# Kernel tuning notes

Hardware: AMD Instinct MI355X
Metric: run time of the kernel (lower is better)

## Reference

```python
import jax, jax.numpy as jnp
import numpy as np

FRAME_PERIOD = 80   # samples per frame
IR_LENGTH = 2000    # filter length L (taps = L-1)
N_FFT = 4096


def setup_inputs() -> dict:
    key = jax.random.key(0)
    k1, k2 = jax.random.split(key)
    x = jax.random.normal(k1, (2, 24000), dtype=jnp.float32)          # waveform, T = 300*80
    mc = jax.random.normal(k2, (2, 300, 25), dtype=jnp.float32) * 0.1  # mel-cepstrum (B, N, M+1)
    return {"x": x, "mc": mc}


def _c2min_phase_ir(c):
    # cepstrum -> minimum-phase impulse response: ifft(exp(fft(c))) truncated.
    # (alpha=0, gamma=0 makes mgc2ir exactly this FFT-based conversion.)
    C = jnp.fft.fft(c, n=N_FFT, axis=-1)
    h = jnp.fft.ifft(jnp.exp(C), axis=-1).real[..., :IR_LENGTH]
    return h


def _linear_interpolate(h):
    # (B, N, L) frame-rate filters -> (B, N*P, L) sample-rate filters,
    # linear interpolation between consecutive frames, last frame replicated.
    B, N, L = h.shape
    P = FRAME_PERIOD
    h_next = jnp.concatenate([h[:, 1:], h[:, -1:]], axis=1)
    w = (jnp.arange(P, dtype=h.dtype) / P)[None, None, :, None]  # (1,1,P,1)
    y = h[:, :, None, :] * (1.0 - w) + h_next[:, :, None, :] * w  # (B,N,P,L)
    return y.reshape(B, N * P, L)


def reference(x, mc):
    L = IR_LENGTH
    h = _c2min_phase_ir(mc)      # (B, N, L) minimum-phase IR
    h = jnp.flip(h, axis=-1)     # phase == 'minimum': flip taps
    h = _linear_interpolate(h)   # (B, T, L)
    T = h.shape[1]
    # causal padding (taps, 0) then unfold into overlapping windows
    x_pad = jnp.pad(x, ((0, 0), (L - 1, 0)))
    idx = jnp.arange(T)[:, None] + jnp.arange(L)[None, :]  # (T, L)
    windows = x_pad[:, idx]                                # (B, T, L)
    y = jnp.sum(windows * h, axis=-1)                      # (B, T)
    return y
```

## Files before the change

### kernel.cpp

```cpp
#include <hip/hip_runtime.h>
#include <math.h>

#define IR_LEN  2000
#define PFRAME  80
#define NFRAMES 300
#define NBATCH  2
#define NROWS   (NBATCH*NFRAMES)
#define T_TOTAL (NFRAMES*PFRAME)
#define NCOEF   25
#define TWO_PI  6.283185307179586f
#define GS      68
#define XWN     2160
#define XWPAD   2432

#define XPHYS(B) ((B) + (((B) >> 5) << 2))

__device__ __forceinline__ void fsincos(float a, float* s, float* c) {
    *s = __sinf(a); *c = __cosf(a);
}

__global__ __launch_bounds__(256) void minphase_fir_fused(
        const float* __restrict__ mc, const float* __restrict__ x,
        float* __restrict__ y) {
    __shared__ __align__(16) float U[8704];
    __shared__ __align__(16) float xws[XWPAD];
    __shared__ float csh[NCOEF];
    float* const EHr = U;
    float* const EHi = U + 4096;
    float* const Gr  = U;
    float* const Gi  = U + 4352;
    float* const hU  = U;
    float* const red = U + 4224;

    const int row   = blockIdx.x;
    const int batch = row / NFRAMES;
    const int frame = row - batch * NFRAMES;
    const int t0    = frame * PFRAME;
    const int t     = threadIdx.x;

    if (t < NCOEF) csh[t] = mc[row * NCOEF + t];

    {
        const float* xb = x + batch * T_TOTAL;
        for (int j = t; j < XWN; j += 256) {
            const int xi = t0 - 2079 + j;
            const float v = (xi >= 0 && xi < T_TOTAL) ? xb[xi] : 0.0f;
            xws[XPHYS(j)] = v;
        }
    }
    __syncthreads();

    {
        float creg[NCOEF];
        #pragma unroll
        for (int k = 0; k < NCOEF; k++) creg[k] = csh[k];

        float bs, bc; fsincos(-(TWO_PI / 4096.0f) * (float)t, &bs, &bc);
        const float SC =  0.923879532511287f;
        const float SS = -0.382683432365090f;
        #pragma unroll 4
        for (int ii = 0; ii < 8; ii++) {
            const int f = t + 256 * ii;
            const float wc = bc, ws = bs;
            { const float nr = bc * SC - bs * SS;
              const float ni = bc * SS + bs * SC;
              bc = nr; bs = ni; }
            const float t2 = 2.0f * wc;
            float b1 = 0.0f, b2 = 0.0f;
            #pragma unroll
            for (int k = NCOEF - 1; k >= 1; k--) {
                const float bk = __fmaf_rn(t2, b1, creg[k] - b2);
                b2 = b1; b1 = bk;
            }
            const float Cr = __fmaf_rn(wc, b1, creg[0] - b2);
            const float Ci = ws * b1;
            const float m = __expf(Cr);
            float si, co; fsincos(Ci, &si, &co);
            const float er = m * co, ei = m * si;
            EHr[f] = er; EHi[f] = ei;
            if (f > 0) { EHr[4096 - f] = er; EHi[4096 - f] = -ei; }
        }
        if (t == 0) {
            float Cr = 0.0f, Ci = 0.0f;
            float cr = 1.0f, ci = 0.0f;
            #pragma unroll
            for (int k = 0; k < NCOEF; k++) {
                Cr += csh[k] * cr; Ci += csh[k] * ci;
                cr = -cr; ci = -ci;
            }
            const float m = __expf(Cr);
            float si, co; fsincos(Ci, &si, &co);
            EHr[2048] = m * co; EHi[2048] = m * si;
        }
    }
    __syncthreads();

    {
        const bool act = t < 144;
        const int bg = t % 9;
        const int dp = t / 9;
        const int b0 = bg * 4;
        const int d0 = dp * 2;
        float Ter[2][4], Tei[2][4], Tor[2][4], Toi[2][4];
        #pragma unroll
        for (int j = 0; j < 2; j++)
            #pragma unroll
            for (int i = 0; i < 4; i++) {
                Ter[j][i] = 0.0f; Tei[j][i] = 0.0f;
                Tor[j][i] = 0.0f; Toi[j][i] = 0.0f;
            }
        float rr[2], ri[2], wr[2], wi[2];
        if (act) {
            #pragma unroll
            for (int j = 0; j < 2; j++) {
                float s, c; fsincos((TWO_PI / 32.0f) * (float)(d0 + j), &s, &c);
                wr[j] = c; wi[j] = s; rr[j] = 1.0f; ri[j] = 0.0f;
            }
            float4 vre = *(const float4*)&EHr[b0];
            float4 vie = *(const float4*)&EHi[b0];
            float4 vro = *(const float4*)&EHr[64 + b0];
            float4 vio = *(const float4*)&EHi[64 + b0];
            #pragma unroll 4
            for (int a2 = 0; a2 < 32; a2++) {
                const float4 cre = vre, cie = vie, cro = vro, cio = vio;
                if (a2 < 31) {
                    const int nb = 128 * (a2 + 1) + b0;
                    vre = *(const float4*)&EHr[nb];
                    vie = *(const float4*)&EHi[nb];
                    vro = *(const float4*)&EHr[nb + 64];
                    vio = *(const float4*)&EHi[nb + 64];
                }
                const float ere[4] = {cre.x, cre.y, cre.z, cre.w};
                const float eie[4] = {cie.x, cie.y, cie.z, cie.w};
                const float ero[4] = {cro.x, cro.y, cro.z, cro.w};
                const float eio[4] = {cio.x, cio.y, cio.z, cio.w};
                #pragma unroll
                for (int j = 0; j < 2; j++) {
                    #pragma unroll
                    for (int i = 0; i < 4; i++) {
                        Ter[j][i] += ere[i] * rr[j] - eie[i] * ri[j];
                        Tei[j][i] += ere[i] * ri[j] + eie[i] * rr[j];
                        Tor[j][i] += ero[i] * rr[j] - eio[i] * ri[j];
                        Toi[j][i] += ero[i] * ri[j] + eio[i] * rr[j];
                    }
                    const float nr = rr[j] * wr[j] - ri[j] * wi[j];
                    const float ni = rr[j] * wi[j] + ri[j] * wr[j];
                    rr[j] = nr; ri[j] = ni;
                }
            }
        }
        __syncthreads();

        if (act) {
            float os[2], oc[2];
            #pragma unroll
            for (int j = 0; j < 2; j++)
                fsincos((TWO_PI / 64.0f) * (float)(d0 + j), &os[j], &oc[j]);
            #pragma unroll
            for (int i = 0; i < 4; i++) {
                const int b = b0 + i;
                if (b > 32) continue;
                float gpr[2], gpi[2], gmr[2], gmi[2];
                #pragma unroll
                for (int j = 0; j < 2; j++) {
                    const int d = d0 + j;
                    const float ur = oc[j] * Tor[j][i] - os[j] * Toi[j][i];
                    const float ui = oc[j] * Toi[j][i] + os[j] * Tor[j][i];
                    const float pr = Ter[j][i] + ur, pi = Tei[j][i] + ui;
                    const float mr = Ter[j][i] - ur, mi = Tei[j][i] - ui;
                    float s, c;
                    fsincos((TWO_PI / 4096.0f) * (float)(b * d), &s, &c);
                    gpr[j] = pr * c - pi * s; gpi[j] = pr * s + pi * c;
                    fsincos((TWO_PI / 4096.0f) * (float)(b * (d + 32)), &s, &c);
                    gmr[j] = mr * c - mi * s; gmi[j] = mr * s + mi * c;
                }
                *(float2*)&Gr[b * GS + d0]      = make_float2(gpr[0], gpr[1]);
                *(float2*)&Gi[b * GS + d0]      = make_float2(gpi[0], gpi[1]);
                *(float2*)&Gr[b * GS + d0 + 32] = make_float2(gmr[0], gmr[1]);
                *(float2*)&Gi[b * GS + d0 + 32] = make_float2(gmi[0], gmi[1]);
            }
        }
    }
    __syncthreads();

    float hv[4][2];
    int   dl_, cg_;
    {
        const int dl = (t & 31) * 2;
        const int cg = t >> 5;
        dl_ = dl; cg_ = cg;
        float swi_, swr_; fsincos((TWO_PI / 64.0f) * (float)cg, &swi_, &swr_);
        const float swr = swr_, swi = swi_;
        float rr = 1.0f, ri = 0.0f;
        float acc00 = 0, acc01 = 0, acc10 = 0, acc11 = 0;
        float acc20 = 0, acc21 = 0, acc30 = 0, acc31 = 0;
        int bb = 0;

#define S2C 0.70710678118654752f
#define STEP2(f8r, f8i, f16r, f16i, f24r, f24i)                                \
        {                                                                      \
            const float2 g_r = *(const float2*)&Gr[bb * GS + dl];              \
            const float2 g_i = *(const float2*)&Gi[bb * GS + dl];              \
            acc00 += g_r.x * rr - g_i.x * ri;                                  \
            acc01 += g_r.y * rr - g_i.y * ri;                                  \
            { const float tr = rr*(f8r) - ri*(f8i), ti = rr*(f8i) + ri*(f8r);  \
              acc10 += g_r.x * tr - g_i.x * ti;                                \
              acc11 += g_r.y * tr - g_i.y * ti; }                              \
            { const float tr = rr*(f16r) - ri*(f16i), ti = rr*(f16i) + ri*(f16r); \
              acc20 += g_r.x * tr - g_i.x * ti;                                \
              acc21 += g_r.y * tr - g_i.y * ti; }                              \
            { const float tr = rr*(f24r) - ri*(f24i), ti = rr*(f24i) + ri*(f24r); \
              acc30 += g_r.x * tr - g_i.x * ti;                                \
              acc31 += g_r.y * tr - g_i.y * ti; }                              \
            { const float nr = rr * swr - ri * swi;                            \
              const float ni = rr * swi + ri * swr;                            \
              rr = nr; ri = ni; }                                              \
            bb++;                                                              \
        }

        #pragma unroll 1
        for (int grp = 0; grp < 4; grp++) {
            STEP2( 1.0f, 0.0f,   1.0f, 0.0f,   1.0f, 0.0f)
            STEP2( S2C,  S2C,    0.0f, 1.0f,  -S2C,  S2C)
            STEP2( 0.0f, 1.0f,  -1.0f, 0.0f,   0.0f,-1.0f)
            STEP2(-S2C,  S2C,    0.0f,-1.0f,   S2C,  S2C)
            STEP2(-1.0f, 0.0f,   1.0f, 0.0f,  -1.0f, 0.0f)
            STEP2(-S2C, -S2C,    0.0f, 1.0f,   S2C, -S2C)
            STEP2( 0.0f,-1.0f,  -1.0f, 0.0f,   0.0f, 1.0f)
            STEP2( S2C, -S2C,    0.0f,-1.0f,  -S2C, -S2C)
        }
#undef STEP2

        const float g0a  = Gr[dl],           g0b  = Gr[dl + 1];
        const float g32a = Gr[32 * GS + dl], g32b = Gr[32 * GS + dl + 1];
        const float sgn  = (cg & 1) ? -1.0f : 1.0f;
        const float sc = 1.0f / 4096.0f;
        hv[0][0] = (2.0f * acc00 - g0a + sgn * g32a) * sc;
        hv[0][1] = (2.0f * acc01 - g0b + sgn * g32b) * sc;
        hv[1][0] = (2.0f * acc10 - g0a + sgn * g32a) * sc;
        hv[1][1] = (2.0f * acc11 - g0b + sgn * g32b) * sc;
        hv[2][0] = (2.0f * acc20 - g0a + sgn * g32a) * sc;
        hv[2][1] = (2.0f * acc21 - g0b + sgn * g32b) * sc;
        hv[3][0] = (2.0f * acc30 - g0a + sgn * g32a) * sc;
        hv[3][1] = (2.0f * acc31 - g0b + sgn * g32b) * sc;
    }
    __syncthreads();

    #pragma unroll
    for (int v = 0; v < 4; v++) {
        const int c = cg_ + 8 * v;
        const int n = 64 * c + dl_;
        if (n < IR_LEN)     hU[n]     = hv[v][0];
        if (n + 1 < IR_LEN) hU[n + 1] = hv[v][1];
    }
    __syncthreads();

    if (t < 240) {
        const int o0 = (t % 20) * 8;
        const int kc = t / 20;
        const int kb = kc * 168;
        const int ns = (kc == 11) ? 38 : 42;
        float s0[8] = {0,0,0,0,0,0,0,0};
        int Bo = o0 + 1996 - kb;
        float4 w1 = *(const float4*)&xws[XPHYS(Bo + 4)];
        float4 w2 = *(const float4*)&xws[XPHYS(Bo + 8)];
        for (int s = 0; s < ns; s++) {
            const float4 w0 = *(const float4*)&xws[XPHYS(Bo)];
            const float4 ha = *(const float4*)&hU[kb + 4 * s];
            const float wv[12] = {w0.x, w0.y, w0.z, w0.w,
                                  w1.x, w1.y, w1.z, w1.w,
                                  w2.x, w2.y, w2.z, w2.w};
            const float hav[4] = {ha.x, ha.y, ha.z, ha.w};
            #pragma unroll
            for (int jo = 0; jo < 8; jo++) {
                #pragma unroll
                for (int jk = 0; jk < 4; jk++) {
                    s0[jo] += hav[jk] * wv[3 + jo - jk];
                }
            }
            w2 = w1; w1 = w0; Bo -= 4;
        }
        const int rb = kc * 168 + o0;
        *(float4*)&red[rb]     = make_float4(s0[0], s0[1], s0[2], s0[3]);
        *(float4*)&red[rb + 4] = make_float4(s0[4], s0[5], s0[6], s0[7]);
    }
    __syncthreads();

    if (t < 160) {
        float z = 0.0f;
        #pragma unroll
        for (int kc = 0; kc < 12; kc++) z += red[kc * 168 + t];
        const int o = t;
        const int tout = t0 - PFRAME + o;
        float wgt = (o < PFRAME) ? (float)o * (1.0f / PFRAME)
                                 : (float)(160 - o) * (1.0f / PFRAME);
        if (frame == NFRAMES - 1 && o >= PFRAME) wgt = 1.0f;
        if (tout >= 0) {
            atomicAdd(&y[batch * T_TOTAL + tout], wgt * z);
        }
    }
}

extern "C" void kernel_launch(void* const* d_in, const int* in_sizes, int n_in,
                              void* d_out, int out_size, void* d_ws, size_t ws_size,
                              hipStream_t stream) {
    const float* x  = (const float*)d_in[0];
    const float* mc = (const float*)d_in[1];
    float* y = (float*)d_out;

    hipMemsetAsync(y, 0, (size_t)out_size * sizeof(float), stream);
    minphase_fir_fused<<<NROWS, 256, 0, stream>>>(mc, x, y);
}
```

Measured before the change: 87.35 us.

## Double block size to 512 threads and halve per-thread work in every stage

Moves the fused kernel from 256 to 512 threads per block and redistributes each phase. The cepstrum FFT loop, the radix stages (one d per thread instead of two, two output columns instead of four) and the FIR tap chunks (24 chunks of 84 taps instead of 12 of 168) are all split across the extra threads. With only 600 blocks spread over the GPU, the intent is more parallelism per frame and shorter serial chains per thread. The cost is a longer final reduction over 24 partial sums and more threads to synchronize at each barrier.

```diff
diff --git a/kernel.cpp b/kernel.cpp
--- a/kernel.cpp
+++ b/kernel.cpp
@@ -19,7 +19,7 @@
     *s = __sinf(a); *c = __cosf(a);
 }
 
-__global__ __launch_bounds__(256) void minphase_fir_fused(
+__global__ __launch_bounds__(512) void minphase_fir_fused(
         const float* __restrict__ mc, const float* __restrict__ x,
         float* __restrict__ y) {
     __shared__ __align__(16) float U[8704];
@@ -42,7 +42,7 @@
 
     {
         const float* xb = x + batch * T_TOTAL;
-        for (int j = t; j < XWN; j += 256) {
+        for (int j = t; j < XWN; j += 512) {
             const int xi = t0 - 2079 + j;
             const float v = (xi >= 0 && xi < T_TOTAL) ? xb[xi] : 0.0f;
             xws[XPHYS(j)] = v;
@@ -56,11 +56,11 @@
         for (int k = 0; k < NCOEF; k++) creg[k] = csh[k];
 
         float bs, bc; fsincos(-(TWO_PI / 4096.0f) * (float)t, &bs, &bc);
-        const float SC =  0.923879532511287f;
-        const float SS = -0.382683432365090f;
+        const float SC =  0.70710678118654752f;
+        const float SS = -0.70710678118654752f;
         #pragma unroll 4
-        for (int ii = 0; ii < 8; ii++) {
-            const int f = t + 256 * ii;
+        for (int ii = 0; ii < 4; ii++) {
+            const int f = t + 512 * ii;
             const float wc = bc, ws = bs;
             { const float nr = bc * SC - bs * SS;
               const float ni = bc * SS + bs * SC;
@@ -96,26 +96,20 @@
     __syncthreads();
 
     {
-        const bool act = t < 144;
+        const bool act = t < 288;
         const int bg = t % 9;
-        const int dp = t / 9;
+        const int d  = t / 9;
         const int b0 = bg * 4;
-        const int d0 = dp * 2;
-        float Ter[2][4], Tei[2][4], Tor[2][4], Toi[2][4];
+        float Ter[4], Tei[4], Tor[4], Toi[4];
         #pragma unroll
-        for (int j = 0; j < 2; j++)
-            #pragma unroll
-            for (int i = 0; i < 4; i++) {
-                Ter[j][i] = 0.0f; Tei[j][i] = 0.0f;
-                Tor[j][i] = 0.0f; Toi[j][i] = 0.0f;
-            }
-        float rr[2], ri[2], wr[2], wi[2];
+        for (int i = 0; i < 4; i++) {
+            Ter[i] = 0.0f; Tei[i] = 0.0f;
+            Tor[i] = 0.0f; Toi[i] = 0.0f;
+        }
+        float rr = 1.0f, ri = 0.0f, wr = 1.0f, wi = 0.0f;
         if (act) {
-            #pragma unroll
-            for (int j = 0; j < 2; j++) {
-                float s, c; fsincos((TWO_PI / 32.0f) * (float)(d0 + j), &s, &c);
-                wr[j] = c; wi[j] = s; rr[j] = 1.0f; ri[j] = 0.0f;
-            }
+            { float s, c; fsincos((TWO_PI / 32.0f) * (float)d, &s, &c);
+              wr = c; wi = s; }
             float4 vre = *(const float4*)&EHr[b0];
             float4 vie = *(const float4*)&EHi[b0];
             float4 vro = *(const float4*)&EHr[64 + b0];
@@ -135,55 +129,42 @@
                 const float ero[4] = {cro.x, cro.y, cro.z, cro.w};
                 const float eio[4] = {cio.x, cio.y, cio.z, cio.w};
                 #pragma unroll
-                for (int j = 0; j < 2; j++) {
-                    #pragma unroll
-                    for (int i = 0; i < 4; i++) {
-                        Ter[j][i] += ere[i] * rr[j] - eie[i] * ri[j];
-                        Tei[j][i] += ere[i] * ri[j] + eie[i] * rr[j];
-                        Tor[j][i] += ero[i] * rr[j] - eio[i] * ri[j];
-                        Toi[j][i] += ero[i] * ri[j] + eio[i] * rr[j];
-                    }
-                    const float nr = rr[j] * wr[j] - ri[j] * wi[j];
-                    const float ni = rr[j] * wi[j] + ri[j] * wr[j];
-                    rr[j] = nr; ri[j] = ni;
+                for (int i = 0; i < 4; i++) {
+                    Ter[i] += ere[i] * rr - eie[i] * ri;
+                    Tei[i] += ere[i] * ri + eie[i] * rr;
+                    Tor[i] += ero[i] * rr - eio[i] * ri;
+                    Toi[i] += ero[i] * ri + eio[i] * rr;
                 }
+                const float nr = rr * wr - ri * wi;
+                const float ni = rr * wi + ri * wr;
+                rr = nr; ri = ni;
             }
         }
         __syncthreads();
 
         if (act) {
-            float os[2], oc[2];
-            #pragma unroll
-            for (int j = 0; j < 2; j++)
-                fsincos((TWO_PI / 64.0f) * (float)(d0 + j), &os[j], &oc[j]);
+            float os, oc; fsincos((TWO_PI / 64.0f) * (float)d, &os, &oc);
             #pragma unroll
             for (int i = 0; i < 4; i++) {
                 const int b = b0 + i;
                 if (b > 32) continue;
-                float gpr[2], gpi[2], gmr[2], gmi[2];
-                #pragma unroll
-                for (int j = 0; j < 2; j++) {
-                    const int d = d0 + j;
-                    const float ur = oc[j] * Tor[j][i] - os[j] * Toi[j][i];
-                    const float ui = oc[j] * Toi[j][i] + os[j] * Tor[j][i];
-                    const float pr = Ter[j][i] + ur, pi = Tei[j][i] + ui;
-                    const float mr = Ter[j][i] - ur, mi = Tei[j][i] - ui;
-                    float s, c;
-                    fsincos((TWO_PI / 4096.0f) * (float)(b * d), &s, &c);
-                    gpr[j] = pr * c - pi * s; gpi[j] = pr * s + pi * c;
-                    fsincos((TWO_PI / 4096.0f) * (float)(b * (d + 32)), &s, &c);
-                    gmr[j] = mr * c - mi * s; gmi[j] = mr * s + mi * c;
-                }
-                *(float2*)&Gr[b * GS + d0]      = make_float2(gpr[0], gpr[1]);
-                *(float2*)&Gi[b * GS + d0]      = make_float2(gpi[0], gpi[1]);
-                *(float2*)&Gr[b * GS + d0 + 32] = make_float2(gmr[0], gmr[1]);
-                *(float2*)&Gi[b * GS + d0 + 32] = make_float2(gmi[0], gmi[1]);
-            }
-        }
-    }
-    __syncthreads();
-
-    float hv[4][2];
+                const float ur = oc * Tor[i] - os * Toi[i];
+                const float ui = oc * Toi[i] + os * Tor[i];
+                const float pr = Ter[i] + ur, pi = Tei[i] + ui;
+                const float mr = Ter[i] - ur, mi = Tei[i] - ui;
+                float s, c;
+                fsincos((TWO_PI / 4096.0f) * (float)(b * d), &s, &c);
+                Gr[b * GS + d]      = pr * c - pi * s;
+                Gi[b * GS + d]      = pr * s + pi * c;
+                fsincos((TWO_PI / 4096.0f) * (float)(b * (d + 32)), &s, &c);
+                Gr[b * GS + d + 32] = mr * c - mi * s;
+                Gi[b * GS + d + 32] = mr * s + mi * c;
+            }
+        }
+    }
+    __syncthreads();
+
+    float hv[2][2];
     int   dl_, cg_;
     {
         const int dl = (t & 31) * 2;
@@ -192,26 +173,18 @@
         float swi_, swr_; fsincos((TWO_PI / 64.0f) * (float)cg, &swi_, &swr_);
         const float swr = swr_, swi = swi_;
         float rr = 1.0f, ri = 0.0f;
-        float acc00 = 0, acc01 = 0, acc10 = 0, acc11 = 0;
-        float acc20 = 0, acc21 = 0, acc30 = 0, acc31 = 0;
+        float acc00 = 0, acc01 = 0, acc20 = 0, acc21 = 0;
         int bb = 0;
 
-#define S2C 0.70710678118654752f
-#define STEP2(f8r, f8i, f16r, f16i, f24r, f24i)                                \
+#define STEP2(f16r, f16i)                                                      \
         {                                                                      \
             const float2 g_r = *(const float2*)&Gr[bb * GS + dl];              \
             const float2 g_i = *(const float2*)&Gi[bb * GS + dl];              \
             acc00 += g_r.x * rr - g_i.x * ri;                                  \
             acc01 += g_r.y * rr - g_i.y * ri;                                  \
-            { const float tr = rr*(f8r) - ri*(f8i), ti = rr*(f8i) + ri*(f8r);  \
-              acc10 += g_r.x * tr - g_i.x * ti;                                \
-              acc11 += g_r.y * tr - g_i.y * ti; }                              \
             { const float tr = rr*(f16r) - ri*(f16i), ti = rr*(f16i) + ri*(f16r); \
               acc20 += g_r.x * tr - g_i.x * ti;                                \
               acc21 += g_r.y * tr - g_i.y * ti; }                              \
-            { const float tr = rr*(f24r) - ri*(f24i), ti = rr*(f24i) + ri*(f24r); \
-              acc30 += g_r.x * tr - g_i.x * ti;                                \
-              acc31 += g_r.y * tr - g_i.y * ti; }                              \
             { const float nr = rr * swr - ri * swi;                            \
               const float ni = rr * swi + ri * swr;                            \
               rr = nr; ri = ni; }                                              \
@@ -220,14 +193,14 @@
 
         #pragma unroll 1
         for (int grp = 0; grp < 4; grp++) {
-            STEP2( 1.0f, 0.0f,   1.0f, 0.0f,   1.0f, 0.0f)
-            STEP2( S2C,  S2C,    0.0f, 1.0f,  -S2C,  S2C)
-            STEP2( 0.0f, 1.0f,  -1.0f, 0.0f,   0.0f,-1.0f)
-            STEP2(-S2C,  S2C,    0.0f,-1.0f,   S2C,  S2C)
-            STEP2(-1.0f, 0.0f,   1.0f, 0.0f,  -1.0f, 0.0f)
-            STEP2(-S2C, -S2C,    0.0f, 1.0f,   S2C, -S2C)
-            STEP2( 0.0f,-1.0f,  -1.0f, 0.0f,   0.0f, 1.0f)
-            STEP2( S2C, -S2C,    0.0f,-1.0f,  -S2C, -S2C)
+            STEP2( 1.0f, 0.0f)
+            STEP2( 0.0f, 1.0f)
+            STEP2(-1.0f, 0.0f)
+            STEP2( 0.0f,-1.0f)
+            STEP2( 1.0f, 0.0f)
+            STEP2( 0.0f, 1.0f)
+            STEP2(-1.0f, 0.0f)
+            STEP2( 0.0f,-1.0f)
         }
 #undef STEP2
 
@@ -237,29 +210,25 @@
         const float sc = 1.0f / 4096.0f;
         hv[0][0] = (2.0f * acc00 - g0a + sgn * g32a) * sc;
         hv[0][1] = (2.0f * acc01 - g0b + sgn * g32b) * sc;
-        hv[1][0] = (2.0f * acc10 - g0a + sgn * g32a) * sc;
-        hv[1][1] = (2.0f * acc11 - g0b + sgn * g32b) * sc;
-        hv[2][0] = (2.0f * acc20 - g0a + sgn * g32a) * sc;
-        hv[2][1] = (2.0f * acc21 - g0b + sgn * g32b) * sc;
-        hv[3][0] = (2.0f * acc30 - g0a + sgn * g32a) * sc;
-        hv[3][1] = (2.0f * acc31 - g0b + sgn * g32b) * sc;
+        hv[1][0] = (2.0f * acc20 - g0a + sgn * g32a) * sc;
+        hv[1][1] = (2.0f * acc21 - g0b + sgn * g32b) * sc;
     }
     __syncthreads();
 
     #pragma unroll
-    for (int v = 0; v < 4; v++) {
-        const int c = cg_ + 8 * v;
+    for (int v = 0; v < 2; v++) {
+        const int c = cg_ + 16 * v;
         const int n = 64 * c + dl_;
         if (n < IR_LEN)     hU[n]     = hv[v][0];
         if (n + 1 < IR_LEN) hU[n + 1] = hv[v][1];
     }
     __syncthreads();
 
-    if (t < 240) {
+    if (t < 480) {
         const int o0 = (t % 20) * 8;
         const int kc = t / 20;
-        const int kb = kc * 168;
-        const int ns = (kc == 11) ? 38 : 42;
+        const int kb = kc * 84;
+        const int ns = (kc == 23) ? 17 : 21;
         float s0[8] = {0,0,0,0,0,0,0,0};
         int Bo = o0 + 1996 - kb;
         float4 w1 = *(const float4*)&xws[XPHYS(Bo + 4)];
@@ -289,7 +258,7 @@
     if (t < 160) {
         float z = 0.0f;
         #pragma unroll
-        for (int kc = 0; kc < 12; kc++) z += red[kc * 168 + t];
+        for (int kc = 0; kc < 24; kc++) z += red[kc * 168 + t];
         const int o = t;
         const int tout = t0 - PFRAME + o;
         float wgt = (o < PFRAME) ? (float)o * (1.0f / PFRAME)
@@ -309,5 +278,5 @@
     float* y = (float*)d_out;
 
     hipMemsetAsync(y, 0, (size_t)out_size * sizeof(float), stream);
-    minphase_fir_fused<<<NROWS, 256, 0, stream>>>(mc, x, y);
+    minphase_fir_fused<<<NROWS, 512, 0, stream>>>(mc, x, y);
 }
```

Result: slower. 106.2 us (+21.6%).

## Split fused min-phase/FIR kernel into IR-generation and FIR-scatter kernels

Applied to the files above, without the earlier changes.

Splits the single fused kernel in two. The first kernel computes each frame's minimum-phase impulse response and writes it to workspace memory. The second kernel launches two blocks per frame, each handling 80 output samples with 25 tap chunks across 250 threads. This raises FIR parallelism and lowers shared-memory use per block in each kernel, which should improve occupancy. The cost is an extra launch plus a global round-trip of the impulse responses, about 4.8 MB written and read back.

```diff
diff --git a/kernel.cpp b/kernel.cpp
--- a/kernel.cpp
+++ b/kernel.cpp
@@ -19,35 +19,20 @@
     *s = __sinf(a); *c = __cosf(a);
 }
 
-__global__ __launch_bounds__(256) void minphase_fir_fused(
-        const float* __restrict__ mc, const float* __restrict__ x,
-        float* __restrict__ y) {
-    __shared__ __align__(16) float U[8704];
-    __shared__ __align__(16) float xws[XWPAD];
+
+__global__ __launch_bounds__(256) void minphase_h(
+        const float* __restrict__ mc, float* __restrict__ hw) {
+    __shared__ __align__(16) float U[8192];
     __shared__ float csh[NCOEF];
     float* const EHr = U;
     float* const EHi = U + 4096;
     float* const Gr  = U;
     float* const Gi  = U + 4352;
-    float* const hU  = U;
-    float* const red = U + 4224;
 
     const int row   = blockIdx.x;
-    const int batch = row / NFRAMES;
-    const int frame = row - batch * NFRAMES;
-    const int t0    = frame * PFRAME;
     const int t     = threadIdx.x;
 
     if (t < NCOEF) csh[t] = mc[row * NCOEF + t];
-
-    {
-        const float* xb = x + batch * T_TOTAL;
-        for (int j = t; j < XWN; j += 256) {
-            const int xi = t0 - 2079 + j;
-            const float v = (xi >= 0 && xi < T_TOTAL) ? xb[xi] : 0.0f;
-            xws[XPHYS(j)] = v;
-        }
-    }
     __syncthreads();
 
     {
@@ -183,12 +168,9 @@
     }
     __syncthreads();
 
-    float hv[4][2];
-    int   dl_, cg_;
     {
         const int dl = (t & 31) * 2;
         const int cg = t >> 5;
-        dl_ = dl; cg_ = cg;
         float swi_, swr_; fsincos((TWO_PI / 64.0f) * (float)cg, &swi_, &swr_);
         const float swr = swr_, swi = swi_;
         float rr = 1.0f, ri = 0.0f;
@@ -235,6 +217,7 @@
         const float g32a = Gr[32 * GS + dl], g32b = Gr[32 * GS + dl + 1];
         const float sgn  = (cg & 1) ? -1.0f : 1.0f;
         const float sc = 1.0f / 4096.0f;
+        float hv[4][2];
         hv[0][0] = (2.0f * acc00 - g0a + sgn * g32a) * sc;
         hv[0][1] = (2.0f * acc01 - g0b + sgn * g32b) * sc;
         hv[1][0] = (2.0f * acc10 - g0a + sgn * g32a) * sc;
@@ -243,30 +226,66 @@
         hv[2][1] = (2.0f * acc21 - g0b + sgn * g32b) * sc;
         hv[3][0] = (2.0f * acc30 - g0a + sgn * g32a) * sc;
         hv[3][1] = (2.0f * acc31 - g0b + sgn * g32b) * sc;
-    }
-    __syncthreads();
-
-    #pragma unroll
-    for (int v = 0; v < 4; v++) {
-        const int c = cg_ + 8 * v;
-        const int n = 64 * c + dl_;
-        if (n < IR_LEN)     hU[n]     = hv[v][0];
-        if (n + 1 < IR_LEN) hU[n + 1] = hv[v][1];
-    }
-    __syncthreads();
-
-    if (t < 240) {
-        const int o0 = (t % 20) * 8;
-        const int kc = t / 20;
-        const int kb = kc * 168;
-        const int ns = (kc == 11) ? 38 : 42;
+
+        float* const hrow = hw + row * IR_LEN;
+        #pragma unroll
+        for (int v = 0; v < 4; v++) {
+            const int c = cg + 8 * v;
+            const int n = 64 * c + dl;
+            if (n + 1 < IR_LEN) {
+                *(float2*)&hrow[n] = make_float2(hv[v][0], hv[v][1]);
+            } else if (n < IR_LEN) {
+                hrow[n] = hv[v][0];
+            }
+        }
+    }
+}
+
+#define BOUT 80
+#define NCH  25
+#define CHL  80
+#define RSTR 88
+
+__global__ __launch_bounds__(256) void fir_scatter(
+        const float* __restrict__ hw, const float* __restrict__ x,
+        float* __restrict__ y) {
+    __shared__ __align__(16) float xws[XWPAD];
+    __shared__ __align__(16) float hh[IR_LEN];
+    __shared__ float red[NCH * RSTR];
+
+    const int bid   = blockIdx.x;
+    const int row   = bid >> 1;
+    const int half  = bid & 1;
+    const int batch = row / NFRAMES;
+    const int frame = row - batch * NFRAMES;
+    const int t0    = frame * PFRAME;
+    const int ob    = half * BOUT;
+    const int t     = threadIdx.x;
+
+    {
+        const float* xb = x + batch * T_TOTAL;
+        for (int j = t; j < XWN; j += 256) {
+            const int xi = t0 - 2079 + j;
+            const float v = (xi >= 0 && xi < T_TOTAL) ? xb[xi] : 0.0f;
+            xws[XPHYS(j)] = v;
+        }
+        const float* hr = hw + row * IR_LEN;
+        for (int j = t; j < IR_LEN; j += 256) hh[j] = hr[j];
+    }
+    __syncthreads();
+
+    if (t < 250) {
+        const int lo0 = (t % 10) * 8;
+        const int o0  = ob + lo0;
+        const int kc  = t / 10;
+        const int kb  = kc * CHL;
         float s0[8] = {0,0,0,0,0,0,0,0};
         int Bo = o0 + 1996 - kb;
         float4 w1 = *(const float4*)&xws[XPHYS(Bo + 4)];
         float4 w2 = *(const float4*)&xws[XPHYS(Bo + 8)];
-        for (int s = 0; s < ns; s++) {
+        for (int s = 0; s < CHL / 4; s++) {
             const float4 w0 = *(const float4*)&xws[XPHYS(Bo)];
-            const float4 ha = *(const float4*)&hU[kb + 4 * s];
+            const float4 ha = *(const float4*)&hh[kb + 4 * s];
             const float wv[12] = {w0.x, w0.y, w0.z, w0.w,
                                   w1.x, w1.y, w1.z, w1.w,
                                   w2.x, w2.y, w2.z, w2.w};
@@ -280,17 +299,17 @@
             }
             w2 = w1; w1 = w0; Bo -= 4;
         }
-        const int rb = kc * 168 + o0;
+        const int rb = kc * RSTR + lo0;
         *(float4*)&red[rb]     = make_float4(s0[0], s0[1], s0[2], s0[3]);
         *(float4*)&red[rb + 4] = make_float4(s0[4], s0[5], s0[6], s0[7]);
     }
     __syncthreads();
 
-    if (t < 160) {
+    if (t < BOUT) {
         float z = 0.0f;
         #pragma unroll
-        for (int kc = 0; kc < 12; kc++) z += red[kc * 168 + t];
-        const int o = t;
+        for (int kc = 0; kc < NCH; kc++) z += red[kc * RSTR + t];
+        const int o = ob + t;
         const int tout = t0 - PFRAME + o;
         float wgt = (o < PFRAME) ? (float)o * (1.0f / PFRAME)
                                  : (float)(160 - o) * (1.0f / PFRAME);
@@ -306,8 +325,10 @@
                               hipStream_t stream) {
     const float* x  = (const float*)d_in[0];
     const float* mc = (const float*)d_in[1];
-    float* y = (float*)d_out;
+    float* y  = (float*)d_out;
+    float* hw = (float*)d_ws;
 
     hipMemsetAsync(y, 0, (size_t)out_size * sizeof(float), stream);
-    minphase_fir_fused<<<NROWS, 256, 0, stream>>>(mc, x, y);
+    minphase_h<<<NROWS, 256, 0, stream>>>(mc, hw);
+    fir_scatter<<<NROWS * 2, 256, 0, stream>>>(hw, x, y);
 }
```

Result: slower. 92.69 us (+6.1%).
